# Optimization experiments

Hardware: AMD Instinct MI355X
Metric: run time of the kernel (lower is better)

## Reference

```python
import jax, jax.numpy as jnp
import numpy as np
from jax import lax

B, N, C, DFF, K = 32, 256, 256, 1024, 8
GRID = 128          # fixed jit-safe eta-phi grid (TF computes it dynamically via reduce_max)
GSIZE = 0.1         # grid_size init kwarg
LN_EPS = 1e-6
BN_EPS = 1e-3       # keras BatchNormalization default epsilon


def setup_inputs() -> dict:
    key = jax.random.key(0)
    ks = jax.random.split(key, 8)
    d = {}
    d['x'] = jax.random.normal(ks[0], (B, N, C), jnp.float32)
    d['coords'] = jax.random.normal(ks[1], (B, N, 2), jnp.float32)
    d['dw_kernel'] = jax.random.normal(ks[2], (K, K, 1, C), jnp.float32) * (1.0 / K)
    d['dw_bias'] = jnp.zeros((C,), jnp.float32)
    d['pw_w'] = jax.random.normal(ks[3], (C, C), jnp.float32) * (1.0 / np.sqrt(C))
    d['pw_b'] = jnp.zeros((C,), jnp.float32)
    d['ln_g'] = jnp.ones((C,), jnp.float32)
    d['ln_b'] = jnp.zeros((C,), jnp.float32)
    d['gi_w1'] = jax.random.normal(ks[4], (C, C), jnp.float32) * (1.0 / np.sqrt(C))
    d['gi_b1'] = jnp.zeros((C,), jnp.float32)
    d['gi_w2'] = jax.random.normal(ks[5], (C, C), jnp.float32) * (1.0 / np.sqrt(C))
    d['gi_b2'] = jnp.zeros((C,), jnp.float32)
    for i in range(3):
        d[f'bn{i}_g'] = jnp.ones((C,), jnp.float32)
        d[f'bn{i}_b'] = jnp.zeros((C,), jnp.float32)
        d[f'bn{i}_m'] = jnp.zeros((C,), jnp.float32)
        d[f'bn{i}_v'] = jnp.ones((C,), jnp.float32)
    d['w_ff1'] = jax.random.normal(ks[6], (C, DFF), jnp.float32) * (1.0 / np.sqrt(C))
    d['b_ff1'] = jnp.zeros((DFF,), jnp.float32)
    d['w_ff2'] = jax.random.normal(ks[7], (DFF, C), jnp.float32) * (1.0 / np.sqrt(DFF))
    d['b_ff2'] = jnp.zeros((C,), jnp.float32)
    return d


def _bn_inf(x, g, b, m, v):
    # keras BatchNormalization, inference path, per-channel (last axis)
    return (x - m) * lax.rsqrt(v + BN_EPS) * g + b


def _layernorm(x, g, b):
    mu = jnp.mean(x, axis=-1, keepdims=True)
    var = jnp.mean(jnp.square(x - mu), axis=-1, keepdims=True)
    return (x - mu) * lax.rsqrt(var + LN_EPS) * g + b


def _forward(x, coords, dw_kernel, dw_bias, pw_w, pw_b, ln_g, ln_b,
             gi_w1, gi_b1, gi_w2, gi_b2,
             bn0_g, bn0_b, bn0_m, bn0_v,
             bn1_g, bn1_b, bn1_m, bn1_v,
             w_ff1, b_ff1, w_ff2, b_ff2,
             bn2_g, bn2_b, bn2_m, bn2_v):
    eta, phi = coords[..., 0], coords[..., 1]

    # ---- GeometricCPE ----
    residual = x
    eta_min = jnp.min(eta, axis=1, keepdims=True)
    phi_min = jnp.min(phi, axis=1, keepdims=True)
    ge = jnp.clip(((eta - eta_min) / GSIZE).astype(jnp.int32), 0, GRID - 1)  # [B,N]
    gp = jnp.clip(((phi - phi_min) / GSIZE).astype(jnp.int32), 0, GRID - 1)
    b_idx = jnp.arange(B)[:, None]                                           # [B,1]

    # scatter-add points into dense grid (tf.scatter_nd sums duplicates)
    grid = jnp.zeros((B, GRID, GRID, C), x.dtype).at[b_idx, ge, gp].add(x)

    # depthwise conv2d, SAME padding (even kernel: lo=3, hi=4 matches TF)
    grid = lax.conv_general_dilated(
        grid, dw_kernel, window_strides=(1, 1), padding='SAME',
        dimension_numbers=('NHWC', 'HWIO', 'NHWC'), feature_group_count=C)
    grid = grid + dw_bias

    out = grid[b_idx, ge, gp]                    # gather back, [B,N,C]
    out = out @ pw_w + pw_b                      # pointwise Dense
    out = _layernorm(out, ln_g, ln_b)
    x = residual + out

    # ---- GlobalInteractionLayer ----
    gctx = jnp.mean(x, axis=1)                   # [B,C]
    y = (gctx @ gi_w1 + gi_b1)[:, None, :] + (x @ gi_w2 + gi_b2)
    y = _bn_inf(y, bn0_g, bn0_b, bn0_m, bn0_v)

    x = _bn_inf(x + y, bn1_g, bn1_b, bn1_m, bn1_v)

    # ---- FFN ----
    y = jax.nn.relu(x @ w_ff1 + b_ff1) @ w_ff2 + b_ff2
    x = _bn_inf(x + y, bn2_g, bn2_b, bn2_m, bn2_v)
    return x


def reference(x, coords, dw_kernel, dw_bias, pw_w, pw_b, ln_g, ln_b,
              gi_w1, gi_b1, gi_w2, gi_b2,
              bn0_g, bn0_b, bn0_m, bn0_v,
              bn1_g, bn1_b, bn1_m, bn1_v,
              w_ff1, b_ff1, w_ff2, b_ff2,
              bn2_g, bn2_b, bn2_m, bn2_v):
    out = _forward(x, coords, dw_kernel, dw_bias, pw_w, pw_b, ln_g, ln_b,
                   gi_w1, gi_b1, gi_w2, gi_b2,
                   bn0_g, bn0_b, bn0_m, bn0_v,
                   bn1_g, bn1_b, bn1_m, bn1_v,
                   w_ff1, b_ff1, w_ff2, b_ff2,
                   bn2_g, bn2_b, bn2_m, bn2_v)
    return (out, coords)
```

## Files before the change

### kernel.cpp

```cpp
#include <hip/hip_runtime.h>
#include <cstdint>
#include <cstddef>

#define B_   32
#define N_   256
#define C_   256
#define DFF_ 1024

typedef unsigned short ushort_t;
typedef __attribute__((ext_vector_type(8))) short bf16x8;
typedef __attribute__((ext_vector_type(4))) float f32x4;

__device__ __forceinline__ ushort_t f2bf(float f) {
    unsigned u = __builtin_bit_cast(unsigned, f);
    u += 0x7FFFu + ((u >> 16) & 1u);
    return (ushort_t)(u >> 16);
}

__device__ __forceinline__ unsigned swz64(unsigned a) {
    return a ^ (((a >> 7) & 7u) << 4);
}

#define GLL(src, dst) __builtin_amdgcn_global_load_lds( \
    (const __attribute__((address_space(1))) void*)(src), \
    (__attribute__((address_space(3))) void*)(dst), 16, 0, 0)

__global__ void k_prep(const float* __restrict__ coords,
                       ushort_t* __restrict__ nbr, int* __restrict__ ncnt,
                       const float* g0, const float* b0, const float* m0, const float* v0,
                       const float* g1, const float* b1, const float* m1, const float* v1,
                       const float* g2, const float* b2, const float* m2, const float* v2,
                       float* __restrict__ sh, float* __restrict__ coords_out,
                       const float* __restrict__ pw, const float* __restrict__ gi,
                       const float* __restrict__ ff1, const float* __restrict__ ff2,
                       ushort_t* __restrict__ tpw, ushort_t* __restrict__ tgi,
                       ushort_t* __restrict__ tff1, ushort_t* __restrict__ tff2) {
    int bid = blockIdx.x;
    if (bid < B_) {
        int b = bid, n = threadIdx.x;
        __shared__ float se[N_], sp[N_];
        __shared__ int sge[N_], sgp[N_];
        float eta = coords[(b * N_ + n) * 2 + 0];
        float phi = coords[(b * N_ + n) * 2 + 1];
        coords_out[b * 512 + n] = coords[b * 512 + n];
        coords_out[b * 512 + 256 + n] = coords[b * 512 + 256 + n];
        se[n] = eta; sp[n] = phi;
        __syncthreads();
        for (int s = 128; s > 0; s >>= 1) {
            if (n < s) {
                se[n] = fminf(se[n], se[n + s]);
                sp[n] = fminf(sp[n], sp[n + s]);
            }
            __syncthreads();
        }
        float emin = se[0], pmin = sp[0];
        int gi2 = (int)((eta - emin) / 0.1f); gi2 = gi2 < 0 ? 0 : (gi2 > 127 ? 127 : gi2);
        int pi = (int)((phi - pmin) / 0.1f); pi = pi < 0 ? 0 : (pi > 127 ? 127 : pi);
        sge[n] = gi2; sgp[n] = pi;
        __syncthreads();
        int cnt = 0;
        ushort_t* out = nbr + ((size_t)b * N_ + n) * N_;
        for (int m = 0; m < N_; ++m) {
            int dh = sge[m] - gi2 + 3;
            int dv = sgp[m] - pi + 3;
            if (((unsigned)dh < 8u) && ((unsigned)dv < 8u))
                out[cnt++] = (ushort_t)(m | ((dh * 8 + dv) << 8));
        }
        ncnt[b * N_ + n] = cnt;
    } else if (bid == B_) {
        int c = threadIdx.x;
        float s;
        s = g0[c] * rsqrtf(v0[c] + 1e-3f); sh[c]        = s; sh[256 + c]  = b0[c] - m0[c] * s;
        s = g1[c] * rsqrtf(v1[c] + 1e-3f); sh[512 + c]  = s; sh[768 + c]  = b1[c] - m1[c] * s;
        s = g2[c] * rsqrtf(v2[c] + 1e-3f); sh[1024 + c] = s; sh[1280 + c] = b2[c] - m2[c] * s;
    } else {
        __shared__ float s[32][33];
        int t2 = bid - (B_ + 1);
        const float* W; ushort_t* T; int K, Nn, t;
        if (t2 < 64)       { W = pw;  T = tpw;  K = 256;  Nn = 256;  t = t2; }
        else if (t2 < 128) { W = gi;  T = tgi;  K = 256;  Nn = 256;  t = t2 - 64; }
        else if (t2 < 384) { W = ff1; T = tff1; K = 256;  Nn = 1024; t = t2 - 128; }
        else               { W = ff2; T = tff2; K = 1024; Nn = 256;  t = t2 - 384; }
        int ntiles_n = Nn >> 5;
        int n0 = (t % ntiles_n) << 5, k0 = (t / ntiles_n) << 5;
        int tx = threadIdx.x & 31, ty = threadIdx.x >> 5;
        #pragma unroll
        for (int j = 0; j < 4; ++j)
            s[ty + j * 8][tx] = W[(size_t)(k0 + ty + j * 8) * Nn + n0 + tx];
        __syncthreads();
        #pragma unroll
        for (int j = 0; j < 4; ++j)
            T[(size_t)(n0 + ty + j * 8) * K + k0 + tx] = f2bf(s[tx][ty + j * 8]);
    }
}

__global__ __launch_bounds__(256) void k_cpe2(
        const float* __restrict__ x,
        const ushort_t* __restrict__ nbr, const int* __restrict__ ncnt,
        const float* __restrict__ dwk, const float* __restrict__ dwb,
        ushort_t* __restrict__ t0) {
    int wv = threadIdx.x >> 6, lane = threadIdx.x & 63;
    int bn = blockIdx.x * 4 + wv;
    int b = bn >> 8;
    int c0 = lane * 4;
    int cnt = ncnt[bn];
    const ushort_t* lst = nbr + (size_t)bn * N_;
    const float* xb = x + (size_t)b * N_ * C_;
    float4 a0 = *(const float4*)(dwb + c0);
    float4 a1 = {0.f, 0.f, 0.f, 0.f};
    float4 a2 = {0.f, 0.f, 0.f, 0.f};
    float4 a3 = {0.f, 0.f, 0.f, 0.f};
    int i = 0;
    for (; i + 4 <= cnt; i += 4) {
        int pk0 = lst[i], pk1 = lst[i + 1], pk2 = lst[i + 2], pk3 = lst[i + 3];
        float4 w0 = *(const float4*)(dwk + (pk0 >> 8) * C_ + c0);
        float4 v0 = *(const float4*)(xb + (pk0 & 255) * C_ + c0);
        float4 w1 = *(const float4*)(dwk + (pk1 >> 8) * C_ + c0);
        float4 v1 = *(const float4*)(xb + (pk1 & 255) * C_ + c0);
        float4 w2 = *(const float4*)(dwk + (pk2 >> 8) * C_ + c0);
        float4 v2 = *(const float4*)(xb + (pk2 & 255) * C_ + c0);
        float4 w3 = *(const float4*)(dwk + (pk3 >> 8) * C_ + c0);
        float4 v3 = *(const float4*)(xb + (pk3 & 255) * C_ + c0);
        a0.x = fmaf(w0.x, v0.x, a0.x); a0.y = fmaf(w0.y, v0.y, a0.y);
        a0.z = fmaf(w0.z, v0.z, a0.z); a0.w = fmaf(w0.w, v0.w, a0.w);
        a1.x = fmaf(w1.x, v1.x, a1.x); a1.y = fmaf(w1.y, v1.y, a1.y);
        a1.z = fmaf(w1.z, v1.z, a1.z); a1.w = fmaf(w1.w, v1.w, a1.w);
        a2.x = fmaf(w2.x, v2.x, a2.x); a2.y = fmaf(w2.y, v2.y, a2.y);
        a2.z = fmaf(w2.z, v2.z, a2.z); a2.w = fmaf(w2.w, v2.w, a2.w);
        a3.x = fmaf(w3.x, v3.x, a3.x); a3.y = fmaf(w3.y, v3.y, a3.y);
        a3.z = fmaf(w3.z, v3.z, a3.z); a3.w = fmaf(w3.w, v3.w, a3.w);
    }
    for (; i < cnt; ++i) {
        int pk = lst[i];
        float4 w = *(const float4*)(dwk + (pk >> 8) * C_ + c0);
        float4 v = *(const float4*)(xb + (pk & 255) * C_ + c0);
        a0.x = fmaf(w.x, v.x, a0.x); a0.y = fmaf(w.y, v.y, a0.y);
        a0.z = fmaf(w.z, v.z, a0.z); a0.w = fmaf(w.w, v.w, a0.w);
    }
    a0.x += a1.x + a2.x + a3.x;
    a0.y += a1.y + a2.y + a3.y;
    a0.z += a1.z + a2.z + a3.z;
    a0.w += a1.w + a2.w + a3.w;
    ushort4 ob; ob.x = f2bf(a0.x); ob.y = f2bf(a0.y); ob.z = f2bf(a0.z); ob.w = f2bf(a0.w);
    *(ushort4*)(t0 + (size_t)bn * C_ + c0) = ob;
}

template <int EPI>
__global__ __launch_bounds__(256) void k_gemmrow(
    const ushort_t* __restrict__ A, const ushort_t* __restrict__ Wt,
    const float* __restrict__ bias,
    ushort_t* __restrict__ Cb, float* __restrict__ Cf,
    const float* __restrict__ residf,
    const float* __restrict__ p0, const float* __restrict__ p1,
    const float* __restrict__ p2, const float* __restrict__ p3,
    float* __restrict__ partial, const float* __restrict__ w1,
    const float* __restrict__ b1) {
    const int K = 256;
    __shared__ __align__(16) ushort_t sA[2][2048];
    __shared__ __align__(16) ushort_t sB[2][16384];
    __shared__ float red[4][32][2];
    __shared__ float sg[C_];
    __shared__ float sgv[C_];
    int tid = threadIdx.x;
    int lane = tid & 63, wv = tid >> 6;
    int rowBase = blockIdx.x * 32;
    int l16 = lane & 15, g = (lane >> 4) & 3;

    unsigned PA = (unsigned)tid * 16;
    unsigned LA = swz64(PA);
    const ushort_t* aSrc = A + (size_t)(rowBase + (LA >> 7)) * K + ((LA >> 1) & 63u);
    const ushort_t* bSrc[8];
    #pragma unroll
    for (int q = 0; q < 8; ++q) {
        unsigned P = q * 4096u + (unsigned)tid * 16;
        unsigned L = swz64(P);
        bSrc[q] = Wt + (size_t)(L >> 7) * K + ((L >> 1) & 63u);
    }
    unsigned wb = (unsigned)(tid >> 6) * 1024;

    unsigned oA[2][2], oB[4][2];
    #pragma unroll
    for (int mi = 0; mi < 2; ++mi)
        #pragma unroll
        for (int kk = 0; kk < 2; ++kk)
            oA[mi][kk] = swz64((unsigned)(((mi * 16 + l16) << 7) + (kk << 6) + (g << 4)));
    #pragma unroll
    for (int ni = 0; ni < 4; ++ni)
        #pragma unroll
        for (int kk = 0; kk < 2; ++kk)
            oB[ni][kk] = swz64((unsigned)(((wv * 64 + ni * 16 + l16) << 7) + (kk << 6) + (g << 4)));

    f32x4 acc[2][4] = {};
    const int nt = K >> 6;

    GLL(aSrc, (char*)sA[0] + wb);
    #pragma unroll
    for (int q = 0; q < 8; ++q) GLL(bSrc[q], (char*)sB[0] + q * 4096 + wb);

    if constexpr (EPI == 2) {
        int j = tid;
        int pb = (blockIdx.x >> 3) << 3;
        float s = 0.f;
        #pragma unroll
        for (int k = 0; k < 8; ++k) s += partial[(size_t)(pb + k) * C_ + j];
        sg[j] = s * (1.f / 256.f);
        __syncthreads();
        float a2 = b1[j];
        #pragma unroll 8
        for (int c2 = 0; c2 < C_; ++c2) a2 = fmaf(sg[c2], w1[c2 * C_ + j], a2);
        sgv[j] = a2;
        __syncthreads();
    }

    int cur = 0;
    for (int t = 0; t < nt; ++t) {
        if (t + 1 < nt) {
            int o = (t + 1) << 6;
            GLL(aSrc + o, (char*)sA[cur ^ 1] + wb);
            #pragma unroll
            for (int q = 0; q < 8; ++q) GLL(bSrc[q] + o, (char*)sB[cur ^ 1] + q * 4096 + wb);
            asm volatile("s_waitcnt vmcnt(9)" ::: "memory");
        } else {
            asm volatile("s_waitcnt vmcnt(0)" ::: "memory");
        }
        asm volatile("s_barrier" ::: "memory");
        const char* cA = (const char*)sA[cur];
        const char* cB = (const char*)sB[cur];
        #pragma unroll
        for (int kk = 0; kk < 2; ++kk) {
            bf16x8 a0 = *(const bf16x8*)(cA + oA[0][kk]);
            bf16x8 a1 = *(const bf16x8*)(cA + oA[1][kk]);
            bf16x8 b0 = *(const bf16x8*)(cB + oB[0][kk]);
            bf16x8 b1v = *(const bf16x8*)(cB + oB[1][kk]);
            bf16x8 b2 = *(const bf16x8*)(cB + oB[2][kk]);
            bf16x8 b3 = *(const bf16x8*)(cB + oB[3][kk]);
            acc[0][0] = __builtin_amdgcn_mfma_f32_16x16x32_bf16(a0, b0, acc[0][0], 0, 0, 0);
            acc[0][1] = __builtin_amdgcn_mfma_f32_16x16x32_bf16(a0, b1v, acc[0][1], 0, 0, 0);
            acc[0][2] = __builtin_amdgcn_mfma_f32_16x16x32_bf16(a0, b2, acc[0][2], 0, 0, 0);
            acc[0][3] = __builtin_amdgcn_mfma_f32_16x16x32_bf16(a0, b3, acc[0][3], 0, 0, 0);
            acc[1][0] = __builtin_amdgcn_mfma_f32_16x16x32_bf16(a1, b0, acc[1][0], 0, 0, 0);
            acc[1][1] = __builtin_amdgcn_mfma_f32_16x16x32_bf16(a1, b1v, acc[1][1], 0, 0, 0);
            acc[1][2] = __builtin_amdgcn_mfma_f32_16x16x32_bf16(a1, b2, acc[1][2], 0, 0, 0);
            acc[1][3] = __builtin_amdgcn_mfma_f32_16x16x32_bf16(a1, b3, acc[1][3], 0, 0, 0);
        }
        asm volatile("s_barrier" ::: "memory");
        cur ^= 1;
    }

    float bv[4];
    #pragma unroll
    for (int ni = 0; ni < 4; ++ni) bv[ni] = bias[wv * 64 + ni * 16 + l16];
    #pragma unroll
    for (int mi = 0; mi < 2; ++mi)
        #pragma unroll
        for (int ni = 0; ni < 4; ++ni)
            #pragma unroll
            for (int j = 0; j < 4; ++j)
                acc[mi][ni][j] += bv[ni];

    if constexpr (EPI == 4) {
        #pragma unroll
        for (int mi = 0; mi < 2; ++mi)
            #pragma unroll
            for (int j = 0; j < 4; ++j) {
                float s = 0.f, q = 0.f;
                #pragma unroll
                for (int ni = 0; ni < 4; ++ni) {
                    float vv = acc[mi][ni][j];
                    s += vv; q += vv * vv;
                }
                #pragma unroll
                for (int off = 1; off < 16; off <<= 1) {
                    s += __shfl_xor(s, off);
                    q += __shfl_xor(q, off);
                }
                if (l16 == 0) {
                    int r = mi * 16 + g * 4 + j;
                    red[wv][r][0] = s;
                    red[wv][r][1] = q;
                }
            }
        __syncthreads();
        float colsum[4] = {0.f, 0.f, 0.f, 0.f};
        #pragma unroll
        for (int mi = 0; mi < 2; ++mi)
            #pragma unroll
            for (int j = 0; j < 4; ++j) {
                int r = mi * 16 + g * 4 + j;
                float sum = red[0][r][0] + red[1][r][0] + red[2][r][0] + red[3][r][0];
                float sq  = red[0][r][1] + red[1][r][1] + red[2][r][1] + red[3][r][1];
                float mu = sum * (1.f / 256.f);
                float var = fmaxf(sq * (1.f / 256.f) - mu * mu, 0.f);
                float rs = rsqrtf(var + 1e-6f);
                int row = rowBase + r;
                #pragma unroll
                for (int ni = 0; ni < 4; ++ni) {
                    int col = wv * 64 + ni * 16 + l16;
                    size_t idx = (size_t)row * C_ + col;
                    float o = residf[idx] + (acc[mi][ni][j] - mu) * rs * p0[col] + p1[col];
                    Cf[idx] = o;
                    Cb[idx] = f2bf(o);
                    colsum[ni] += o;
                }
            }
        #pragma unroll
        for (int ni = 0; ni < 4; ++ni) {
            float s = colsum[ni];
            s += __shfl_xor(s, 16);
            s += __shfl_xor(s, 32);
            if (g == 0) partial[(size_t)blockIdx.x * C_ + wv * 64 + ni * 16 + l16] = s;
        }
    } else {
        #pragma unroll
        for (int ni = 0; ni < 4; ++ni) {
            int col = wv * 64 + ni * 16 + l16;
            float gv = sgv[col];
            float s0v = p0[col], h0v = p1[col], s1v = p2[col], h1v = p3[col];
            #pragma unroll
            for (int mi = 0; mi < 2; ++mi)
                #pragma unroll
                for (int j = 0; j < 4; ++j) {
                    int row = rowBase + mi * 16 + g * 4 + j;
                    size_t idx = (size_t)row * C_ + col;
                    float v = acc[mi][ni][j] + gv;
                    v = v * s0v + h0v;
                    float o = (residf[idx] + v) * s1v + h1v;
                    Cf[idx] = o;
                    Cb[idx] = f2bf(o);
                }
        }
    }
}

template <int EPI, int BN>
__global__ __launch_bounds__(256) void k_gemm128(
    const ushort_t* __restrict__ A, const ushort_t* __restrict__ Wt,
    const float* __restrict__ bias, int K, int Nn,
    ushort_t* __restrict__ Cb, float* __restrict__ Cf,
    const float* __restrict__ residf,
    const float* __restrict__ p0, const float* __restrict__ p1) {
    const int NI = BN / 32;
    const int QB = BN / 32;
    __shared__ __align__(16) ushort_t sA[2][8192];
    __shared__ __align__(16) ushort_t sB[2][BN * 64];
    int tid = threadIdx.x;
    int lane = tid & 63, wv = tid >> 6;
    int rowBase = blockIdx.y * 128, colBase = blockIdx.x * BN;
    int l16 = lane & 15, g = (lane >> 4) & 3;
    int wr = (wv >> 1) * 64, wc = (wv & 1) * (BN / 2);

    const ushort_t* aSrc[4];
    #pragma unroll
    for (int q = 0; q < 4; ++q) {
        unsigned P = q * 4096u + (unsigned)tid * 16;
        unsigned L = swz64(P);
        aSrc[q] = A + (size_t)(rowBase + (L >> 7)) * K + ((L >> 1) & 63u);
    }
    const ushort_t* bSrc[QB];
    #pragma unroll
    for (int q = 0; q < QB; ++q) {
        unsigned P = q * 4096u + (unsigned)tid * 16;
        unsigned L = swz64(P);
        bSrc[q] = Wt + (size_t)(colBase + (L >> 7)) * K + ((L >> 1) & 63u);
    }
    unsigned wb = (unsigned)(tid >> 6) * 1024;

    unsigned oA[4][2], oB[NI][2];
    #pragma unroll
    for (int mi = 0; mi < 4; ++mi)
        #pragma unroll
        for (int kk = 0; kk < 2; ++kk)
            oA[mi][kk] = swz64((unsigned)(((wr + mi * 16 + l16) << 7) + (kk << 6) + (g << 4)));
    #pragma unroll
    for (int ni = 0; ni < NI; ++ni)
        #pragma unroll
        for (int kk = 0; kk < 2; ++kk)
            oB[ni][kk] = swz64((unsigned)(((wc + ni * 16 + l16) << 7) + (kk << 6) + (g << 4)));

    f32x4 acc[4][NI] = {};
    int nt = K >> 6;

    #pragma unroll
    for (int q = 0; q < 4; ++q) GLL(aSrc[q], (char*)sA[0] + q * 4096 + wb);
    #pragma unroll
    for (int q = 0; q < QB; ++q) GLL(bSrc[q], (char*)sB[0] + q * 4096 + wb);

    int cur = 0;
    for (int t = 0; t < nt; ++t) {
        if (t + 1 < nt) {
            int o = (t + 1) << 6;
            #pragma unroll
            for (int q = 0; q < 4; ++q) GLL(aSrc[q] + o, (char*)sA[cur ^ 1] + q * 4096 + wb);
            #pragma unroll
            for (int q = 0; q < QB; ++q) GLL(bSrc[q] + o, (char*)sB[cur ^ 1] + q * 4096 + wb);
            if constexpr (BN == 128) asm volatile("s_waitcnt vmcnt(8)" ::: "memory");
            else                     asm volatile("s_waitcnt vmcnt(6)" ::: "memory");
        } else {
            asm volatile("s_waitcnt vmcnt(0)" ::: "memory");
        }
        asm volatile("s_barrier" ::: "memory");
        const char* cA = (const char*)sA[cur];
        const char* cB = (const char*)sB[cur];
        #pragma unroll
        for (int kk = 0; kk < 2; ++kk) {
            bf16x8 af[4], bff[NI];
            #pragma unroll
            for (int mi = 0; mi < 4; ++mi) af[mi] = *(const bf16x8*)(cA + oA[mi][kk]);
            #pragma unroll
            for (int ni = 0; ni < NI; ++ni) bff[ni] = *(const bf16x8*)(cB + oB[ni][kk]);
            #pragma unroll
            for (int mi = 0; mi < 4; ++mi)
                #pragma unroll
                for (int ni = 0; ni < NI; ++ni)
                    acc[mi][ni] = __builtin_amdgcn_mfma_f32_16x16x32_bf16(af[mi], bff[ni], acc[mi][ni], 0, 0, 0);
        }
        asm volatile("s_barrier" ::: "memory");
        cur ^= 1;
    }

    #pragma unroll
    for (int ni = 0; ni < NI; ++ni) {
        int col = colBase + wc + ni * 16 + l16;
        float bvv = bias[col];
        float s0v = 0.f, h0v = 0.f;
        if constexpr (EPI == 3) { s0v = p0[col]; h0v = p1[col]; }
        #pragma unroll
        for (int mi = 0; mi < 4; ++mi)
            #pragma unroll
            for (int j = 0; j < 4; ++j) {
                int row = rowBase + wr + mi * 16 + g * 4 + j;
                size_t idx = (size_t)row * Nn + col;
                float v = acc[mi][ni][j] + bvv;
                if constexpr (EPI == 1) {
                    Cb[idx] = f2bf(fmaxf(v, 0.f));
                } else {
                    Cf[idx] = (residf[idx] + v) * s0v + h0v;
                }
            }
    }
}

extern "C" void kernel_launch(void* const* d_in, const int* in_sizes, int n_in,
                              void* d_out, int out_size, void* d_ws, size_t ws_size,
                              hipStream_t stream) {
    const float* x      = (const float*)d_in[0];
    const float* coords = (const float*)d_in[1];
    const float* dwk    = (const float*)d_in[2];
    const float* dwb    = (const float*)d_in[3];
    const float* pw_w   = (const float*)d_in[4];
    const float* pw_b   = (const float*)d_in[5];
    const float* ln_g   = (const float*)d_in[6];
    const float* ln_b   = (const float*)d_in[7];
    const float* gi_w1  = (const float*)d_in[8];
    const float* gi_b1  = (const float*)d_in[9];
    const float* gi_w2  = (const float*)d_in[10];
    const float* gi_b2  = (const float*)d_in[11];
    const float* bn0g = (const float*)d_in[12], *bn0b = (const float*)d_in[13];
    const float* bn0m = (const float*)d_in[14], *bn0v = (const float*)d_in[15];
    const float* bn1g = (const float*)d_in[16], *bn1b = (const float*)d_in[17];
    const float* bn1m = (const float*)d_in[18], *bn1v = (const float*)d_in[19];
    const float* bn2g = (const float*)d_in[20], *bn2b = (const float*)d_in[21];
    const float* bn2m = (const float*)d_in[22], *bn2v = (const float*)d_in[23];
    const float* w_ff1 = (const float*)d_in[24];
    const float* b_ff1 = (const float*)d_in[25];
    const float* w_ff2 = (const float*)d_in[26];
    const float* b_ff2 = (const float*)d_in[27];

    char* ws = (char*)d_ws;
    int*      ncnt    = (int*)(ws + 0);
    float*    bnsh    = (float*)(ws + 32768);
    float*    partial = (float*)(ws + 40960);
    ushort_t* WtPW    = (ushort_t*)(ws + 303104);
    ushort_t* WtGI    = (ushort_t*)(ws + 434176);
    ushort_t* WtF1    = (ushort_t*)(ws + 565248);
    ushort_t* WtF2    = (ushort_t*)(ws + 1089536);
    ushort_t* nbr     = (ushort_t*)(ws + 1613824);
    float*    x1f     = (float*)(ws + 5808128);
    ushort_t* x1b     = (ushort_t*)(ws + 14196736);
    float*    x2f     = (float*)(ws + 18391040);
    ushort_t* x2b     = (ushort_t*)(ws + 26779648);
    ushort_t* u_b     = (ushort_t*)(ws + 30973952);
    ushort_t* t0      = u_b;
    float*    outx    = (float*)d_out;

    const int M = B_ * N_;

    k_prep<<<B_ + 1 + 640, 256, 0, stream>>>(
        coords, nbr, ncnt,
        bn0g, bn0b, bn0m, bn0v, bn1g, bn1b, bn1m, bn1v, bn2g, bn2b, bn2m, bn2v,
        bnsh, outx + (size_t)M * C_,
        pw_w, gi_w2, w_ff1, w_ff2, WtPW, WtGI, WtF1, WtF2);

    k_cpe2<<<M / 4, 256, 0, stream>>>(x, nbr, ncnt, dwk, dwb, t0);

    k_gemmrow<4><<<M / 32, 256, 0, stream>>>(
        t0, WtPW, pw_b, x1b, x1f,
        x, ln_g, ln_b, nullptr, nullptr,
        partial, nullptr, nullptr);

    k_gemmrow<2><<<M / 32, 256, 0, stream>>>(
        x1b, WtGI, gi_b2, x2b, x2f,
        x1f, bnsh, bnsh + 256, bnsh + 512, bnsh + 768,
        partial, gi_w1, gi_b1);

    k_gemm128<1, 128><<<dim3(DFF_ / 128, M / 128), 256, 0, stream>>>(
        x2b, WtF1, b_ff1, C_, DFF_, u_b, nullptr, nullptr, nullptr, nullptr);

    k_gemm128<3, 64><<<dim3(C_ / 64, M / 128), 256, 0, stream>>>(
        u_b, WtF2, b_ff2, DFF_, C_, nullptr, outx,
        x2f, bnsh + 1024, bnsh + 1280);
}
```

Baseline: 103.4 us.

## Drop fp32 residual copies, use bf16 residuals and 512-thread row GEMMs

The two row-GEMM kernels no longer write fp32 copies of the intermediate activations; later residual adds read the bf16 copies, cutting global traffic. The row GEMMs move to 512 threads with 8 waves each covering 32 columns, and the whole A tile is loaded into LDS once while only B is double-buffered. The gctx matvec in the GI kernel is split across two thread halves. Reading residuals in bf16 instead of fp32 reduces precision.

Result: faster. 94.97 us (-8.1%).

```diff
diff --git a/kernel.cpp b/kernel.cpp
--- a/kernel.cpp
+++ b/kernel.cpp
@@ -15,6 +15,9 @@
     unsigned u = __builtin_bit_cast(unsigned, f);
     u += 0x7FFFu + ((u >> 16) & 1u);
     return (ushort_t)(u >> 16);
+}
+__device__ __forceinline__ float bf2f(ushort_t b) {
+    return __builtin_bit_cast(float, (unsigned)b << 16);
 }
 
 __device__ __forceinline__ unsigned swz64(unsigned a) {
@@ -146,114 +149,120 @@
 }
 
 template <int EPI>
-__global__ __launch_bounds__(256) void k_gemmrow(
+__global__ __launch_bounds__(512) void k_gemmrow8(
     const ushort_t* __restrict__ A, const ushort_t* __restrict__ Wt,
     const float* __restrict__ bias,
-    ushort_t* __restrict__ Cb, float* __restrict__ Cf,
-    const float* __restrict__ residf,
+    ushort_t* __restrict__ Cb,
+    const float* __restrict__ residf, const ushort_t* __restrict__ residb,
     const float* __restrict__ p0, const float* __restrict__ p1,
     const float* __restrict__ p2, const float* __restrict__ p3,
     float* __restrict__ partial, const float* __restrict__ w1,
     const float* __restrict__ b1) {
     const int K = 256;
-    __shared__ __align__(16) ushort_t sA[2][2048];
+    __shared__ __align__(16) ushort_t sA[8192];
     __shared__ __align__(16) ushort_t sB[2][16384];
-    __shared__ float red[4][32][2];
+    __shared__ float red[8][32][2];
     __shared__ float sg[C_];
+    __shared__ float sgp[2][C_];
     __shared__ float sgv[C_];
-    int tid = threadIdx.x;
-    int lane = tid & 63, wv = tid >> 6;
+    int tid = threadIdx.x, lane = tid & 63, wv = tid >> 6;
     int rowBase = blockIdx.x * 32;
     int l16 = lane & 15, g = (lane >> 4) & 3;
 
-    unsigned PA = (unsigned)tid * 16;
-    unsigned LA = swz64(PA);
-    const ushort_t* aSrc = A + (size_t)(rowBase + (LA >> 7)) * K + ((LA >> 1) & 63u);
-    const ushort_t* bSrc[8];
-    #pragma unroll
-    for (int q = 0; q < 8; ++q) {
-        unsigned P = q * 4096u + (unsigned)tid * 16;
+    const ushort_t* aSrc[2];
+    unsigned aOff[2];
+    #pragma unroll
+    for (int q = 0; q < 2; ++q) {
+        unsigned P = q * 8192u + (unsigned)tid * 16u;
         unsigned L = swz64(P);
-        bSrc[q] = Wt + (size_t)(L >> 7) * K + ((L >> 1) & 63u);
-    }
-    unsigned wb = (unsigned)(tid >> 6) * 1024;
-
-    unsigned oA[2][2], oB[4][2];
+        unsigned chunk = L >> 12;
+        unsigned row = (L >> 7) & 31u;
+        unsigned k = (L & 127u) >> 1;
+        aSrc[q] = A + (size_t)(rowBase + row) * K + chunk * 64 + k;
+        aOff[q] = q * 8192u + (unsigned)wv * 1024u;
+    }
+    const ushort_t* bSrc[4];
+    unsigned bOff[4];
+    #pragma unroll
+    for (int q = 0; q < 4; ++q) {
+        unsigned P = q * 8192u + (unsigned)tid * 16u;
+        unsigned L = swz64(P);
+        bSrc[q] = Wt + (size_t)(L >> 7) * K + ((L & 127u) >> 1);
+        bOff[q] = q * 8192u + (unsigned)wv * 1024u;
+    }
+    #pragma unroll
+    for (int q = 0; q < 2; ++q) GLL(aSrc[q], (char*)sA + aOff[q]);
+    #pragma unroll
+    for (int q = 0; q < 4; ++q) GLL(bSrc[q], (char*)sB[0] + bOff[q]);
+
+    if constexpr (EPI == 2) {
+        int j = tid & 255, h = tid >> 8;
+        if (h == 0) {
+            int pb = (blockIdx.x >> 3) << 3;
+            float s = 0.f;
+            #pragma unroll
+            for (int k2 = 0; k2 < 8; ++k2) s += partial[(size_t)(pb + k2) * C_ + j];
+            sg[j] = s * (1.f / 256.f);
+        }
+        __syncthreads();
+        float a2 = 0.f;
+        #pragma unroll 8
+        for (int c2 = h * 128; c2 < h * 128 + 128; ++c2)
+            a2 = fmaf(sg[c2], w1[c2 * C_ + j], a2);
+        sgp[h][j] = a2;
+        __syncthreads();
+        if (h == 0) sgv[j] = b1[j] + sgp[0][j] + sgp[1][j];
+        __syncthreads();
+    }
+
+    unsigned oA[2][2], oB[2][2];
     #pragma unroll
     for (int mi = 0; mi < 2; ++mi)
         #pragma unroll
         for (int kk = 0; kk < 2; ++kk)
             oA[mi][kk] = swz64((unsigned)(((mi * 16 + l16) << 7) + (kk << 6) + (g << 4)));
     #pragma unroll
-    for (int ni = 0; ni < 4; ++ni)
+    for (int ni = 0; ni < 2; ++ni)
         #pragma unroll
         for (int kk = 0; kk < 2; ++kk)
-            oB[ni][kk] = swz64((unsigned)(((wv * 64 + ni * 16 + l16) << 7) + (kk << 6) + (g << 4)));
-
-    f32x4 acc[2][4] = {};
-    const int nt = K >> 6;
-
-    GLL(aSrc, (char*)sA[0] + wb);
-    #pragma unroll
-    for (int q = 0; q < 8; ++q) GLL(bSrc[q], (char*)sB[0] + q * 4096 + wb);
-
-    if constexpr (EPI == 2) {
-        int j = tid;
-        int pb = (blockIdx.x >> 3) << 3;
-        float s = 0.f;
-        #pragma unroll
-        for (int k = 0; k < 8; ++k) s += partial[(size_t)(pb + k) * C_ + j];
-        sg[j] = s * (1.f / 256.f);
-        __syncthreads();
-        float a2 = b1[j];
-        #pragma unroll 8
-        for (int c2 = 0; c2 < C_; ++c2) a2 = fmaf(sg[c2], w1[c2 * C_ + j], a2);
-        sgv[j] = a2;
-        __syncthreads();
-    }
-
+            oB[ni][kk] = swz64((unsigned)(((wv * 32 + ni * 16 + l16) << 7) + (kk << 6) + (g << 4)));
+
+    f32x4 acc[2][2] = {};
     int cur = 0;
-    for (int t = 0; t < nt; ++t) {
-        if (t + 1 < nt) {
+    for (int t = 0; t < 4; ++t) {
+        if (t < 3) {
             int o = (t + 1) << 6;
-            GLL(aSrc + o, (char*)sA[cur ^ 1] + wb);
-            #pragma unroll
-            for (int q = 0; q < 8; ++q) GLL(bSrc[q] + o, (char*)sB[cur ^ 1] + q * 4096 + wb);
-            asm volatile("s_waitcnt vmcnt(9)" ::: "memory");
+            #pragma unroll
+            for (int q = 0; q < 4; ++q) GLL(bSrc[q] + o, (char*)sB[cur ^ 1] + bOff[q]);
+            asm volatile("s_waitcnt vmcnt(4)" ::: "memory");
         } else {
             asm volatile("s_waitcnt vmcnt(0)" ::: "memory");
         }
         asm volatile("s_barrier" ::: "memory");
-        const char* cA = (const char*)sA[cur];
+        const char* cA = (const char*)sA + t * 4096;
         const char* cB = (const char*)sB[cur];
         #pragma unroll
         for (int kk = 0; kk < 2; ++kk) {
-            bf16x8 a0 = *(const bf16x8*)(cA + oA[0][kk]);
-            bf16x8 a1 = *(const bf16x8*)(cA + oA[1][kk]);
-            bf16x8 b0 = *(const bf16x8*)(cB + oB[0][kk]);
+            bf16x8 a0v = *(const bf16x8*)(cA + oA[0][kk]);
+            bf16x8 a1v = *(const bf16x8*)(cA + oA[1][kk]);
+            bf16x8 b0v = *(const bf16x8*)(cB + oB[0][kk]);
             bf16x8 b1v = *(const bf16x8*)(cB + oB[1][kk]);
-            bf16x8 b2 = *(const bf16x8*)(cB + oB[2][kk]);
-            bf16x8 b3 = *(const bf16x8*)(cB + oB[3][kk]);
-            acc[0][0] = __builtin_amdgcn_mfma_f32_16x16x32_bf16(a0, b0, acc[0][0], 0, 0, 0);
-            acc[0][1] = __builtin_amdgcn_mfma_f32_16x16x32_bf16(a0, b1v, acc[0][1], 0, 0, 0);
-            acc[0][2] = __builtin_amdgcn_mfma_f32_16x16x32_bf16(a0, b2, acc[0][2], 0, 0, 0);
-            acc[0][3] = __builtin_amdgcn_mfma_f32_16x16x32_bf16(a0, b3, acc[0][3], 0, 0, 0);
-            acc[1][0] = __builtin_amdgcn_mfma_f32_16x16x32_bf16(a1, b0, acc[1][0], 0, 0, 0);
-            acc[1][1] = __builtin_amdgcn_mfma_f32_16x16x32_bf16(a1, b1v, acc[1][1], 0, 0, 0);
-            acc[1][2] = __builtin_amdgcn_mfma_f32_16x16x32_bf16(a1, b2, acc[1][2], 0, 0, 0);
-            acc[1][3] = __builtin_amdgcn_mfma_f32_16x16x32_bf16(a1, b3, acc[1][3], 0, 0, 0);
+            acc[0][0] = __builtin_amdgcn_mfma_f32_16x16x32_bf16(a0v, b0v, acc[0][0], 0, 0, 0);
+            acc[0][1] = __builtin_amdgcn_mfma_f32_16x16x32_bf16(a0v, b1v, acc[0][1], 0, 0, 0);
+            acc[1][0] = __builtin_amdgcn_mfma_f32_16x16x32_bf16(a1v, b0v, acc[1][0], 0, 0, 0);
+            acc[1][1] = __builtin_amdgcn_mfma_f32_16x16x32_bf16(a1v, b1v, acc[1][1], 0, 0, 0);
         }
         asm volatile("s_barrier" ::: "memory");
         cur ^= 1;
     }
 
-    float bv[4];
-    #pragma unroll
-    for (int ni = 0; ni < 4; ++ni) bv[ni] = bias[wv * 64 + ni * 16 + l16];
+    float bv[2];
+    #pragma unroll
+    for (int ni = 0; ni < 2; ++ni) bv[ni] = bias[wv * 32 + ni * 16 + l16];
     #pragma unroll
     for (int mi = 0; mi < 2; ++mi)
         #pragma unroll
-        for (int ni = 0; ni < 4; ++ni)
+        for (int ni = 0; ni < 2; ++ni)
             #pragma unroll
             for (int j = 0; j < 4; ++j)
                 acc[mi][ni][j] += bv[ni];
@@ -263,12 +272,8 @@
         for (int mi = 0; mi < 2; ++mi)
             #pragma unroll
             for (int j = 0; j < 4; ++j) {
-                float s = 0.f, q = 0.f;
-                #pragma unroll
-                for (int ni = 0; ni < 4; ++ni) {
-                    float vv = acc[mi][ni][j];
-                    s += vv; q += vv * vv;
-                }
+                float s = acc[mi][0][j] + acc[mi][1][j];
+                float q = acc[mi][0][j] * acc[mi][0][j] + acc[mi][1][j] * acc[mi][1][j];
                 #pragma unroll
                 for (int off = 1; off < 16; off <<= 1) {
                     s += __shfl_xor(s, off);
@@ -281,39 +286,40 @@
                 }
             }
         __syncthreads();
-        float colsum[4] = {0.f, 0.f, 0.f, 0.f};
+        float colsum[2] = {0.f, 0.f};
         #pragma unroll
         for (int mi = 0; mi < 2; ++mi)
             #pragma unroll
             for (int j = 0; j < 4; ++j) {
                 int r = mi * 16 + g * 4 + j;
-                float sum = red[0][r][0] + red[1][r][0] + red[2][r][0] + red[3][r][0];
-                float sq  = red[0][r][1] + red[1][r][1] + red[2][r][1] + red[3][r][1];
+                float sum = 0.f, sq = 0.f;
+                #pragma unroll
+                for (int w = 0; w < 8; ++w) { sum += red[w][r][0]; sq += red[w][r][1]; }
                 float mu = sum * (1.f / 256.f);
                 float var = fmaxf(sq * (1.f / 256.f) - mu * mu, 0.f);
                 float rs = rsqrtf(var + 1e-6f);
                 int row = rowBase + r;
                 #pragma unroll
-                for (int ni = 0; ni < 4; ++ni) {
-                    int col = wv * 64 + ni * 16 + l16;
+                for (int ni = 0; ni < 2; ++ni) {
+                    int col = wv * 32 + ni * 16 + l16;
                     size_t idx = (size_t)row * C_ + col;
                     float o = residf[idx] + (acc[mi][ni][j] - mu) * rs * p0[col] + p1[col];
-                    Cf[idx] = o;
                     Cb[idx] = f2bf(o);
                     colsum[ni] += o;
                 }
             }
         #pragma unroll
-        for (int ni = 0; ni < 4; ++ni) {
+        for (int ni = 0; ni < 2; ++ni) {
             float s = colsum[ni];
             s += __shfl_xor(s, 16);
             s += __shfl_xor(s, 32);
-            if (g == 0) partial[(size_t)blockIdx.x * C_ + wv * 64 + ni * 16 + l16] = s;
+            if (g == 0) partial[(size_t)blockIdx.x * C_ + wv * 32 + ni * 16 + l16] = s;
         }
     } else {
         #pragma unroll
-        for (int ni = 0; ni < 4; ++ni) {
-            int col = wv * 64 + ni * 16 + l16;
+        for (int ni = 0; ni < 2; ++ni) {
+            int col = wv * 32 + ni * 16 + l16;
+            float bvv = bv[ni];
             float gv = sgv[col];
             float s0v = p0[col], h0v = p1[col], s1v = p2[col], h1v = p3[col];
             #pragma unroll
@@ -324,8 +330,7 @@
                     size_t idx = (size_t)row * C_ + col;
                     float v = acc[mi][ni][j] + gv;
                     v = v * s0v + h0v;
-                    float o = (residf[idx] + v) * s1v + h1v;
-                    Cf[idx] = o;
+                    float o = (bf2f(residb[idx]) + v) * s1v + h1v;
                     Cb[idx] = f2bf(o);
                 }
         }
@@ -337,7 +342,7 @@
     const ushort_t* __restrict__ A, const ushort_t* __restrict__ Wt,
     const float* __restrict__ bias, int K, int Nn,
     ushort_t* __restrict__ Cb, float* __restrict__ Cf,
-    const float* __restrict__ residf,
+    const ushort_t* __restrict__ residb,
     const float* __restrict__ p0, const float* __restrict__ p1) {
     const int NI = BN / 32;
     const int QB = BN / 32;
@@ -434,7 +439,7 @@
                 if constexpr (EPI == 1) {
                     Cb[idx] = f2bf(fmaxf(v, 0.f));
                 } else {
-                    Cf[idx] = (residf[idx] + v) * s0v + h0v;
+                    Cf[idx] = (bf2f(residb[idx]) + v) * s0v + h0v;
                 }
             }
     }
@@ -475,12 +480,10 @@
     ushort_t* WtF1    = (ushort_t*)(ws + 565248);
     ushort_t* WtF2    = (ushort_t*)(ws + 1089536);
     ushort_t* nbr     = (ushort_t*)(ws + 1613824);
-    float*    x1f     = (float*)(ws + 5808128);
-    ushort_t* x1b     = (ushort_t*)(ws + 14196736);
-    float*    x2f     = (float*)(ws + 18391040);
-    ushort_t* x2b     = (ushort_t*)(ws + 26779648);
-    ushort_t* u_b     = (ushort_t*)(ws + 30973952);
-    ushort_t* t0      = u_b;
+    ushort_t* x1b     = (ushort_t*)(ws + 5808128);
+    ushort_t* x2b     = (ushort_t*)(ws + 10002432);
+    ushort_t* t0      = (ushort_t*)(ws + 14196736);
+    ushort_t* u_b     = (ushort_t*)(ws + 18391040);
     float*    outx    = (float*)d_out;
 
     const int M = B_ * N_;
@@ -493,20 +496,20 @@
 
     k_cpe2<<<M / 4, 256, 0, stream>>>(x, nbr, ncnt, dwk, dwb, t0);
 
-    k_gemmrow<4><<<M / 32, 256, 0, stream>>>(
-        t0, WtPW, pw_b, x1b, x1f,
-        x, ln_g, ln_b, nullptr, nullptr,
+    k_gemmrow8<4><<<M / 32, 512, 0, stream>>>(
+        t0, WtPW, pw_b, x1b, x, nullptr,
+        ln_g, ln_b, nullptr, nullptr,
         partial, nullptr, nullptr);
 
-    k_gemmrow<2><<<M / 32, 256, 0, stream>>>(
-        x1b, WtGI, gi_b2, x2b, x2f,
-        x1f, bnsh, bnsh + 256, bnsh + 512, bnsh + 768,
+    k_gemmrow8<2><<<M / 32, 512, 0, stream>>>(
+        x1b, WtGI, gi_b2, x2b, nullptr, x1b,
+        bnsh, bnsh + 256, bnsh + 512, bnsh + 768,
         partial, gi_w1, gi_b1);
 
     k_gemm128<1, 128><<<dim3(DFF_ / 128, M / 128), 256, 0, stream>>>(
         x2b, WtF1, b_ff1, C_, DFF_, u_b, nullptr, nullptr, nullptr, nullptr);
 
     k_gemm128<3, 64><<<dim3(C_ / 64, M / 128), 256, 0, stream>>>(
-        u_b, WtF2, b_ff2, DFF_, C_, nullptr, outx,
-        x2f, bnsh + 1024, bnsh + 1280);
-}
+        u_b, WtF2, b_ff2, DFF_, C_, nullptr, outx, x2b,
+        bnsh + 1024, bnsh + 1280);
+}
```
